# Performance work log

Hardware: AMD Instinct MI355X
Metric: run time of the kernel (lower is better)

The kernel has to match this reference:

```python
import jax, jax.numpy as jnp
import numpy as np
import math

IN_DIM = 128
OUT_DIM = 128
EDGE_DIM = 16
LN_EPS = 1e-5


def setup_inputs() -> dict:
    key = jax.random.key(0)
    ks = jax.random.split(key, 6)
    bs, N = 8, 512
    x = jax.random.normal(ks[0], (bs, N, IN_DIM), dtype=jnp.float32)
    edge_feats = jax.random.normal(ks[1], (bs, N, N, EDGE_DIM), dtype=jnp.float32)
    # fc weight (out_dim, in_dim), xavier-uniform scale
    lim_w = math.sqrt(6.0 / (IN_DIM + OUT_DIM))
    W = jax.random.uniform(ks[2], (OUT_DIM, IN_DIM), minval=-lim_w, maxval=lim_w, dtype=jnp.float32)
    # attn_fc weight (1, 2*out_dim+edge_dim) split into a_src | a_dst | a_e
    fan_in = 2 * OUT_DIM + EDGE_DIM
    lim_a = math.sqrt(6.0 / (fan_in + 1))
    a = jax.random.uniform(ks[3], (fan_in,), minval=-lim_a, maxval=lim_a, dtype=jnp.float32)
    a_src, a_dst, a_e = a[:OUT_DIM], a[OUT_DIM:2 * OUT_DIM], a[2 * OUT_DIM:]
    gamma = jnp.ones((OUT_DIM,), dtype=jnp.float32)
    beta = jnp.zeros((OUT_DIM,), dtype=jnp.float32)
    return {"x": x, "edge_feats": edge_feats, "W": W, "a_src": a_src,
            "a_dst": a_dst, "a_e": a_e, "gamma": gamma, "beta": beta}


def reference(x, edge_feats, W, a_src, a_dst, a_e, gamma, beta):
    # h: (bs, N, out_dim)
    h = jnp.einsum('bni,oi->bno', x, W)
    scale = 1.0 / math.sqrt(OUT_DIM)
    # Decomposed rank-1 attention score: attn_fc([h_i, h_j, e_ij]) =
    # h_i.a_src + h_j.a_dst + e_ij.a_e  -- identical math, no (bs,N,N,2D+E) tensor.
    s_i = jnp.einsum('bnd,d->bn', h, a_src)           # row term (index i)
    s_j = jnp.einsum('bnd,d->bn', h, a_dst)           # col term (index j)
    s_e = jnp.einsum('bije,e->bij', edge_feats, a_e)  # edge term
    e_ij = (s_i[:, :, None] + s_j[:, None, :] + s_e) * scale  # (bs, N, N)
    # max-subtract then softmax over j (jax.nn.softmax is already max-stable,
    # and softmax(e - max) == softmax(e))
    alpha = jax.nn.softmax(e_ij, axis=-1)
    # weighted sum over neighbors j (dropout skipped: eval mode)
    h_prime = jnp.einsum('bij,bjd->bid', alpha, h)
    # LayerNorm over last dim
    mu = jnp.mean(h_prime, axis=-1, keepdims=True)
    var = jnp.var(h_prime, axis=-1, keepdims=True)
    out = (h_prime - mu) * jax.lax.rsqrt(var + LN_EPS) * gamma + beta
    return out
```

## Files before the change

kernel.cpp:

```cpp
#include <hip/hip_runtime.h>
#include <math.h>

#define NB 8
#define NN 512
#define D 128
#define TI 8
#define K1R 8
#define LN_EPS 1e-5f
#define SCALE 0.08838834764831845f

#define KE_BLOCKS 2048
#define KE_NTH (KE_BLOCKS * 256)
#define TOT_F4 (NB * NN * NN * 4)

typedef float f32x4 __attribute__((ext_vector_type(4)));

__device__ __forceinline__ float dotv(f32x4 a, f32x4 b) {
    f32x4 m = a * b;
    return m.x + m.y + m.z + m.w;
}
__device__ __forceinline__ float dot4(float4 a, float4 b) {
    return a.x * b.x + a.y * b.y + a.z * b.z + a.w * b.w;
}

__global__ __launch_bounds__(256) void ke_scores(
    const float* __restrict__ ef, const float* __restrict__ a_e,
    float* __restrict__ se_ws)
{
    const int g = blockIdx.x * 256 + threadIdx.x;
    const int c = g & 3;
    const f32x4 A = ((const f32x4*)a_e)[c];
    const f32x4* ef4 = (const f32x4*)ef;
#pragma unroll 4
    for (int k = 0; k < TOT_F4 / KE_NTH; ++k) {
        const size_t f = (size_t)k * KE_NTH + g;
        const f32x4 v = ef4[f];
        float p = dotv(v, A);
        p += __shfl_xor(p, 1);
        p += __shfl_xor(p, 2);
        if (c == 0) se_ws[f >> 2] = p;
    }
}

__global__ __launch_bounds__(256) void k1_proj(
    const float* __restrict__ x, const float* __restrict__ W,
    const float* __restrict__ a_src, const float* __restrict__ a_dst,
    float* __restrict__ h_ws, float* __restrict__ si_ws, float* __restrict__ sj_ws)
{
    __shared__ __align__(16) float4 Wl[128][32];
    __shared__ __align__(16) float4 xl[K1R][32];
    __shared__ float redk[K1R][2][2];

    const int t = threadIdx.x;
    const int row0 = blockIdx.x * K1R;

    const float4* Wg = (const float4*)W;
#pragma unroll
    for (int k = 0; k < 16; ++k) {
        const int f = t + 256 * k;
        const int o = f >> 5, q = f & 31;
        Wl[o][q ^ (o & 7)] = Wg[f];
    }
    xl[t >> 5][t & 31] = ((const float4*)(x + (size_t)row0 * D))[t];
    __syncthreads();

    const int o = t & 127;
    const int rb = (t >> 7) * (K1R / 2);
    float acc[K1R / 2] = {0.f, 0.f, 0.f, 0.f};
#pragma unroll
    for (int q = 0; q < 32; ++q) {
        const float4 wv = Wl[o][q ^ (o & 7)];
#pragma unroll
        for (int r = 0; r < K1R / 2; ++r) acc[r] += dot4(wv, xl[rb + r][q]);
    }
    const float as = a_src[o], ad = a_dst[o];
#pragma unroll
    for (int r = 0; r < K1R / 2; ++r) {
        h_ws[(size_t)(row0 + rb + r) * D + o] = acc[r];
        float vs = acc[r] * as, vd = acc[r] * ad;
#pragma unroll
        for (int m = 32; m >= 1; m >>= 1) {
            vs += __shfl_xor(vs, m);
            vd += __shfl_xor(vd, m);
        }
        if ((t & 63) == 0) {
            redk[rb + r][0][(t >> 6) & 1] = vs;
            redk[rb + r][1][(t >> 6) & 1] = vd;
        }
    }
    __syncthreads();
    if (t < K1R) si_ws[row0 + t] = redk[t][0][0] + redk[t][0][1];
    else if (t < 2 * K1R) {
        const int r = t - K1R;
        sj_ws[row0 + r] = redk[r][1][0] + redk[r][1][1];
    }
}

__global__ __launch_bounds__(512) void k2_attn(
    const float* __restrict__ se_ws,
    const float* __restrict__ gamma, const float* __restrict__ beta,
    const float* __restrict__ h_ws, const float* __restrict__ si_ws,
    const float* __restrict__ sj_ws, float* __restrict__ out)
{
    __shared__ float sj_l[NN];
    __shared__ __align__(16) float alpha[TI][NN];
    __shared__ __align__(16) float part[8][TI][D];
    __shared__ float redm[TI][2];
    __shared__ float reds[TI][2];

    const int t = threadIdx.x;
    const int w = t >> 6;
    const int lane = t & 63;
    const int bid = blockIdx.x;
    const int b = bid >> 6;
    const int i0 = (bid & 63) << 3;

    sj_l[t] = sj_ws[b * NN + t];
    __syncthreads();

    const int q = t & 127;
    const int rg = t >> 7;
    const int r0 = rg * 2, r1 = rg * 2 + 1;
    const int wh = (t >> 6) & 1;
    const float si0 = si_ws[b * NN + i0 + r0];
    const float si1 = si_ws[b * NN + i0 + r1];
    const f32x4 se0 = *(const f32x4*)(se_ws + ((size_t)b * NN + i0 + r0) * NN + 4 * q);
    const f32x4 se1 = *(const f32x4*)(se_ws + ((size_t)b * NN + i0 + r1) * NN + 4 * q);
    const f32x4 sjv = *(const f32x4*)&sj_l[4 * q];
    const f32x4 e0 = (si0 + sjv + se0) * SCALE;
    const f32x4 e1 = (si1 + sjv + se1) * SCALE;
    float m0 = fmaxf(fmaxf(e0.x, e0.y), fmaxf(e0.z, e0.w));
    float m1 = fmaxf(fmaxf(e1.x, e1.y), fmaxf(e1.z, e1.w));
#pragma unroll
    for (int mm = 32; mm >= 1; mm >>= 1) {
        m0 = fmaxf(m0, __shfl_xor(m0, mm));
        m1 = fmaxf(m1, __shfl_xor(m1, mm));
    }
    if (lane == 0) { redm[r0][wh] = m0; redm[r1][wh] = m1; }
    __syncthreads();

    {
        const float mx0 = fmaxf(redm[r0][0], redm[r0][1]);
        const float mx1 = fmaxf(redm[r1][0], redm[r1][1]);
        f32x4 a0, a1;
        a0.x = __expf(e0.x - mx0); a0.y = __expf(e0.y - mx0);
        a0.z = __expf(e0.z - mx0); a0.w = __expf(e0.w - mx0);
        a1.x = __expf(e1.x - mx1); a1.y = __expf(e1.y - mx1);
        a1.z = __expf(e1.z - mx1); a1.w = __expf(e1.w - mx1);
        *(f32x4*)&alpha[r0][4 * q] = a0;
        *(f32x4*)&alpha[r1][4 * q] = a1;
        float s0 = a0.x + a0.y + a0.z + a0.w;
        float s1 = a1.x + a1.y + a1.z + a1.w;
#pragma unroll
        for (int mm = 32; mm >= 1; mm >>= 1) {
            s0 += __shfl_xor(s0, mm);
            s1 += __shfl_xor(s1, mm);
        }
        if (lane == 0) { reds[r0][wh] = s0; reds[r1][wh] = s1; }
    }
    __syncthreads();

    const int dl = (t & 31) << 2;
    const int g = t >> 5;
    float acc[TI][4];
#pragma unroll
    for (int r = 0; r < TI; ++r)
#pragma unroll
        for (int c = 0; c < 4; ++c) acc[r][c] = 0.f;

    const float* hb = h_ws + (size_t)b * NN * D;
#pragma unroll 2
    for (int jt = 0; jt < 8; ++jt) {
        const int j0 = (g << 5) + (jt << 2);
        float4 hv0 = *(const float4*)(hb + (size_t)(j0 + 0) * D + dl);
        float4 hv1 = *(const float4*)(hb + (size_t)(j0 + 1) * D + dl);
        float4 hv2 = *(const float4*)(hb + (size_t)(j0 + 2) * D + dl);
        float4 hv3 = *(const float4*)(hb + (size_t)(j0 + 3) * D + dl);
#pragma unroll
        for (int r = 0; r < TI; ++r) {
            const f32x4 av = *(const f32x4*)&alpha[r][j0];
            acc[r][0] += av.x * hv0.x + av.y * hv1.x + av.z * hv2.x + av.w * hv3.x;
            acc[r][1] += av.x * hv0.y + av.y * hv1.y + av.z * hv2.y + av.w * hv3.y;
            acc[r][2] += av.x * hv0.z + av.y * hv1.z + av.z * hv2.z + av.w * hv3.z;
            acc[r][3] += av.x * hv0.w + av.y * hv1.w + av.z * hv2.w + av.w * hv3.w;
        }
    }
#pragma unroll
    for (int r = 0; r < TI; ++r)
#pragma unroll
        for (int c = 0; c < 4; ++c) acc[r][c] += __shfl_xor(acc[r][c], 32);
    if (lane < 32) {
#pragma unroll
        for (int r = 0; r < TI; ++r)
            *(float4*)&part[w][r][dl] = make_float4(acc[r][0], acc[r][1], acc[r][2], acc[r][3]);
    }
    __syncthreads();

    {
        const int r = w;
        const float inv = 1.0f / (reds[r][0] + reds[r][1]);
        const int d0 = lane, d1 = lane + 64;
        float v0 = 0.f, v1 = 0.f;
#pragma unroll
        for (int pw = 0; pw < 8; ++pw) {
            v0 += part[pw][r][d0];
            v1 += part[pw][r][d1];
        }
        v0 *= inv; v1 *= inv;
        float s = v0 + v1, qq = v0 * v0 + v1 * v1;
#pragma unroll
        for (int mm = 32; mm >= 1; mm >>= 1) {
            s += __shfl_xor(s, mm);
            qq += __shfl_xor(qq, mm);
        }
        const float mu = s * (1.f / 128.f);
        const float var = qq * (1.f / 128.f) - mu * mu;
        const float rs = rsqrtf(var + LN_EPS);
        const size_t ob = ((size_t)(b * NN + i0 + r)) * D;
        out[ob + d0] = (v0 - mu) * rs * gamma[d0] + beta[d0];
        out[ob + d1] = (v1 - mu) * rs * gamma[d1] + beta[d1];
    }
}

extern "C" void kernel_launch(void* const* d_in, const int* in_sizes, int n_in,
                              void* d_out, int out_size, void* d_ws, size_t ws_size,
                              hipStream_t stream) {
    const float* x     = (const float*)d_in[0];
    const float* ef    = (const float*)d_in[1];
    const float* W     = (const float*)d_in[2];
    const float* a_src = (const float*)d_in[3];
    const float* a_dst = (const float*)d_in[4];
    const float* a_e   = (const float*)d_in[5];
    const float* gamma = (const float*)d_in[6];
    const float* beta  = (const float*)d_in[7];
    float* out = (float*)d_out;

    float* h_ws  = (float*)d_ws;
    float* si_ws = h_ws + (size_t)NB * NN * D;
    float* sj_ws = si_ws + NB * NN;
    float* se_ws = (float*)((char*)d_ws + (4u << 20));

    ke_scores<<<KE_BLOCKS, 256, 0, stream>>>(ef, a_e, se_ws);
    k1_proj<<<NB * NN / K1R, 256, 0, stream>>>(x, W, a_src, a_dst, h_ws, si_ws, sj_ws);
    k2_attn<<<NB * (NN / TI), 512, 0, stream>>>(se_ws, gamma, beta,
                                                h_ws, si_ws, sj_ws, out);
}
```

Baseline: 59.13 us.

## Fuse edge-score reduction into attention kernel, dropping the se workspace round trip

Removes the separate edge-score kernel and computes the edge dot products from edge_feats directly inside the attention kernel, writing them into shared memory that is then reused for the softmax weights. This avoids writing and re-reading the 8 MB score workspace and one kernel launch. The attention tile shrinks from 8 to 4 rows per block with 256 threads, doubling the block count and the number of h reloads per row, and the edge-feature streaming now has to overlap with the compute phases inside each block.

New measurement: 55.43 us. 1.07x faster.

```diff
diff --git a/kernel.cpp b/kernel.cpp
--- a/kernel.cpp
+++ b/kernel.cpp
@@ -4,15 +4,11 @@
 #define NB 8
 #define NN 512
 #define D 128
-#define TI 8
+#define TIF 4
 #define K1R 8
 #define LN_EPS 1e-5f
 #define SCALE 0.08838834764831845f
 
-#define KE_BLOCKS 2048
-#define KE_NTH (KE_BLOCKS * 256)
-#define TOT_F4 (NB * NN * NN * 4)
-
 typedef float f32x4 __attribute__((ext_vector_type(4)));
 
 __device__ __forceinline__ float dotv(f32x4 a, f32x4 b) {
@@ -21,25 +17,6 @@
 }
 __device__ __forceinline__ float dot4(float4 a, float4 b) {
     return a.x * b.x + a.y * b.y + a.z * b.z + a.w * b.w;
-}
-
-__global__ __launch_bounds__(256) void ke_scores(
-    const float* __restrict__ ef, const float* __restrict__ a_e,
-    float* __restrict__ se_ws)
-{
-    const int g = blockIdx.x * 256 + threadIdx.x;
-    const int c = g & 3;
-    const f32x4 A = ((const f32x4*)a_e)[c];
-    const f32x4* ef4 = (const f32x4*)ef;
-#pragma unroll 4
-    for (int k = 0; k < TOT_F4 / KE_NTH; ++k) {
-        const size_t f = (size_t)k * KE_NTH + g;
-        const f32x4 v = ef4[f];
-        float p = dotv(v, A);
-        p += __shfl_xor(p, 1);
-        p += __shfl_xor(p, 2);
-        if (c == 0) se_ws[f >> 2] = p;
-    }
 }
 
 __global__ __launch_bounds__(256) void k1_proj(
@@ -96,39 +73,52 @@
     }
 }
 
-__global__ __launch_bounds__(512) void k2_attn(
-    const float* __restrict__ se_ws,
+__global__ __launch_bounds__(256, 4) void kfused(
+    const float* __restrict__ ef, const float* __restrict__ a_e,
     const float* __restrict__ gamma, const float* __restrict__ beta,
     const float* __restrict__ h_ws, const float* __restrict__ si_ws,
     const float* __restrict__ sj_ws, float* __restrict__ out)
 {
     __shared__ float sj_l[NN];
-    __shared__ __align__(16) float alpha[TI][NN];
-    __shared__ __align__(16) float part[8][TI][D];
-    __shared__ float redm[TI][2];
-    __shared__ float reds[TI][2];
+    __shared__ __align__(16) float sa[TIF][NN];
+    __shared__ __align__(16) float part[4][TIF][D];
+    __shared__ float redm[TIF][2];
+    __shared__ float reds[TIF][2];
 
     const int t = threadIdx.x;
     const int w = t >> 6;
     const int lane = t & 63;
     const int bid = blockIdx.x;
-    const int b = bid >> 6;
-    const int i0 = (bid & 63) << 3;
+    const int b = bid >> 7;
+    const int i0 = (bid & 127) * TIF;
 
     sj_l[t] = sj_ws[b * NN + t];
+    sj_l[t + 256] = sj_ws[b * NN + t + 256];
+
+    const int c = t & 3;
+    const f32x4 A = ((const f32x4*)a_e)[c];
+    const f32x4* ef4 = (const f32x4*)ef + ((size_t)b * NN + i0) * NN * 4;
+    float* saf = &sa[0][0];
+#pragma unroll 8
+    for (int k = 0; k < 32; ++k) {
+        const int f = 256 * k + t;
+        const f32x4 v = ef4[f];
+        float p = dotv(v, A);
+        p += __shfl_xor(p, 1);
+        p += __shfl_xor(p, 2);
+        if (c == 0) saf[f >> 2] = p;
+    }
     __syncthreads();
 
     const int q = t & 127;
-    const int rg = t >> 7;
-    const int r0 = rg * 2, r1 = rg * 2 + 1;
+    const int rp = t >> 7;
+    const int r0 = 2 * rp, r1 = 2 * rp + 1;
     const int wh = (t >> 6) & 1;
     const float si0 = si_ws[b * NN + i0 + r0];
     const float si1 = si_ws[b * NN + i0 + r1];
-    const f32x4 se0 = *(const f32x4*)(se_ws + ((size_t)b * NN + i0 + r0) * NN + 4 * q);
-    const f32x4 se1 = *(const f32x4*)(se_ws + ((size_t)b * NN + i0 + r1) * NN + 4 * q);
     const f32x4 sjv = *(const f32x4*)&sj_l[4 * q];
-    const f32x4 e0 = (si0 + sjv + se0) * SCALE;
-    const f32x4 e1 = (si1 + sjv + se1) * SCALE;
+    const f32x4 e0 = (si0 + sjv + *(const f32x4*)&sa[r0][4 * q]) * SCALE;
+    const f32x4 e1 = (si1 + sjv + *(const f32x4*)&sa[r1][4 * q]) * SCALE;
     float m0 = fmaxf(fmaxf(e0.x, e0.y), fmaxf(e0.z, e0.w));
     float m1 = fmaxf(fmaxf(e1.x, e1.y), fmaxf(e1.z, e1.w));
 #pragma unroll
@@ -147,8 +137,8 @@
         a0.z = __expf(e0.z - mx0); a0.w = __expf(e0.w - mx0);
         a1.x = __expf(e1.x - mx1); a1.y = __expf(e1.y - mx1);
         a1.z = __expf(e1.z - mx1); a1.w = __expf(e1.w - mx1);
-        *(f32x4*)&alpha[r0][4 * q] = a0;
-        *(f32x4*)&alpha[r1][4 * q] = a1;
+        *(f32x4*)&sa[r0][4 * q] = a0;
+        *(f32x4*)&sa[r1][4 * q] = a1;
         float s0 = a0.x + a0.y + a0.z + a0.w;
         float s1 = a1.x + a1.y + a1.z + a1.w;
 #pragma unroll
@@ -162,23 +152,23 @@
 
     const int dl = (t & 31) << 2;
     const int g = t >> 5;
-    float acc[TI][4];
-#pragma unroll
-    for (int r = 0; r < TI; ++r)
-#pragma unroll
-        for (int c = 0; c < 4; ++c) acc[r][c] = 0.f;
+    float acc[TIF][4];
+#pragma unroll
+    for (int r = 0; r < TIF; ++r)
+#pragma unroll
+        for (int cc = 0; cc < 4; ++cc) acc[r][cc] = 0.f;
 
     const float* hb = h_ws + (size_t)b * NN * D;
 #pragma unroll 2
-    for (int jt = 0; jt < 8; ++jt) {
-        const int j0 = (g << 5) + (jt << 2);
+    for (int jt = 0; jt < 16; ++jt) {
+        const int j0 = (g << 6) + (jt << 2);
         float4 hv0 = *(const float4*)(hb + (size_t)(j0 + 0) * D + dl);
         float4 hv1 = *(const float4*)(hb + (size_t)(j0 + 1) * D + dl);
         float4 hv2 = *(const float4*)(hb + (size_t)(j0 + 2) * D + dl);
         float4 hv3 = *(const float4*)(hb + (size_t)(j0 + 3) * D + dl);
 #pragma unroll
-        for (int r = 0; r < TI; ++r) {
-            const f32x4 av = *(const f32x4*)&alpha[r][j0];
+        for (int r = 0; r < TIF; ++r) {
+            const f32x4 av = *(const f32x4*)&sa[r][j0];
             acc[r][0] += av.x * hv0.x + av.y * hv1.x + av.z * hv2.x + av.w * hv3.x;
             acc[r][1] += av.x * hv0.y + av.y * hv1.y + av.z * hv2.y + av.w * hv3.y;
             acc[r][2] += av.x * hv0.z + av.y * hv1.z + av.z * hv2.z + av.w * hv3.z;
@@ -186,12 +176,12 @@
         }
     }
 #pragma unroll
-    for (int r = 0; r < TI; ++r)
-#pragma unroll
-        for (int c = 0; c < 4; ++c) acc[r][c] += __shfl_xor(acc[r][c], 32);
+    for (int r = 0; r < TIF; ++r)
+#pragma unroll
+        for (int cc = 0; cc < 4; ++cc) acc[r][cc] += __shfl_xor(acc[r][cc], 32);
     if (lane < 32) {
 #pragma unroll
-        for (int r = 0; r < TI; ++r)
+        for (int r = 0; r < TIF; ++r)
             *(float4*)&part[w][r][dl] = make_float4(acc[r][0], acc[r][1], acc[r][2], acc[r][3]);
     }
     __syncthreads();
@@ -202,7 +192,7 @@
         const int d0 = lane, d1 = lane + 64;
         float v0 = 0.f, v1 = 0.f;
 #pragma unroll
-        for (int pw = 0; pw < 8; ++pw) {
+        for (int pw = 0; pw < 4; ++pw) {
             v0 += part[pw][r][d0];
             v1 += part[pw][r][d1];
         }
@@ -238,10 +228,8 @@
     float* h_ws  = (float*)d_ws;
     float* si_ws = h_ws + (size_t)NB * NN * D;
     float* sj_ws = si_ws + NB * NN;
-    float* se_ws = (float*)((char*)d_ws + (4u << 20));
-
-    ke_scores<<<KE_BLOCKS, 256, 0, stream>>>(ef, a_e, se_ws);
+
     k1_proj<<<NB * NN / K1R, 256, 0, stream>>>(x, W, a_src, a_dst, h_ws, si_ws, sj_ws);
-    k2_attn<<<NB * (NN / TI), 512, 0, stream>>>(se_ws, gamma, beta,
-                                                h_ws, si_ws, sj_ws, out);
-}
+    kfused<<<NB * NN / TIF, 256, 0, stream>>>(ef, a_e, gamma, beta,
+                                              h_ws, si_ws, sj_ws, out);
+}
```
